# Performance work log

Measured on AMD Instinct MI355X. Metric: run time of the kernel, lower is better.

## Reference

```python
import jax, jax.numpy as jnp
import numpy as np


def _layernorm(x, g, b, eps=1e-5):
    m = jnp.mean(x, axis=-1, keepdims=True)
    v = jnp.var(x, axis=-1, keepdims=True)
    return (x - m) / jnp.sqrt(v + eps) * g + b


def _gat_layer(x, W, a1, a2, Wo, bo, diag_mask):
    # x: [B,N,D]; W: [H,D,D]; a1,a2: [H,D]; Wo: [H*D,D]; bo: [D]
    # Additive-attention split: a.[h_i;h_j] = a1.h_i + a2.h_j (same math as
    # the torch concat+linear, since the score layer is linear and bias-free).
    h = jnp.einsum('bni,hio->bhno', x, W)                       # [B,H,N,D]
    s1 = jnp.einsum('bhnd,hd->bhn', h, a1)                      # [B,H,N]
    s2 = jnp.einsum('bhnd,hd->bhn', h, a2)                      # [B,H,N]
    e = jax.nn.leaky_relu(s1[..., :, None] + s2[..., None, :], 0.2)  # [B,H,N,N]
    # fully-connected adjacency = ones - eye -> mask only the diagonal
    e = jnp.where(diag_mask, -jnp.inf, e)
    alpha = jax.nn.softmax(e, axis=-1)                          # [B,H,N,N]
    out = jnp.einsum('bhij,bhjd->bhid', alpha, h)               # [B,H,N,D]
    B, H, N, D = out.shape
    out = out.transpose(0, 2, 1, 3).reshape(B, N, H * D)        # concat heads
    return out @ Wo + bo                                        # [B,N,D]


def setup_inputs() -> dict:
    key = jax.random.key(0)
    ks = jax.random.split(key, 9)
    B, N, IN, D, H, L = 16, 1024, 7, 128, 4, 3
    s = 0.1
    return {
        'node_features': jax.random.normal(ks[0], (B, N, IN), jnp.float32),
        'Wp': jax.random.normal(ks[1], (IN, D), jnp.float32) * s,
        'bp': jax.random.normal(ks[2], (D,), jnp.float32) * s,
        'W':  jax.random.normal(ks[3], (L, H, D, D), jnp.float32) * s,
        'a1': jax.random.normal(ks[4], (L, H, D), jnp.float32) * s,
        'a2': jax.random.normal(ks[5], (L, H, D), jnp.float32) * s,
        'Wo': jax.random.normal(ks[6], (L, H * D, D), jnp.float32) * s,
        'bo': jax.random.normal(ks[7], (L, D), jnp.float32) * s,
        'gamma': jnp.ones((L, D), jnp.float32),
        'beta': jnp.zeros((L, D), jnp.float32),
    }


def reference(node_features, Wp, bp, W, a1, a2, Wo, bo, gamma, beta):
    B, N, _ = node_features.shape
    L = W.shape[0]
    diag_mask = jnp.eye(N, dtype=bool)  # adjacency==0 positions of (ones-eye)
    x = node_features @ Wp + bp         # input_proj
    for i in range(L):
        x_new = _gat_layer(x, W[i], a1[i], a2[i], Wo[i], bo[i], diag_mask)
        if i > 0:
            x = _layernorm(x + x_new, gamma[i], beta[i])  # residual + LN
        else:
            x = _layernorm(x_new, gamma[i], beta[i])
        if i < L - 1:
            x = jax.nn.relu(x)
    return x
```

## Files before the change

kernel.cpp:

```cpp
#include <hip/hip_runtime.h>
#include <hip/hip_bf16.h>

typedef __attribute__((ext_vector_type(8))) _Float16 f16x8;
typedef __attribute__((ext_vector_type(2))) _Float16 f16x2;
typedef __attribute__((ext_vector_type(8))) short short8;
typedef __attribute__((ext_vector_type(4))) short short4v;
typedef __attribute__((ext_vector_type(4))) float f32x4;

#define LDP 72
#define LDH 64

typedef const __attribute__((address_space(1))) unsigned int* gas_ptr;
typedef __attribute__((address_space(3))) unsigned int* las_ptr;
#define GLDS16(gp, lp) \
  __builtin_amdgcn_global_load_lds((gas_ptr)(gp), (las_ptr)(lp), 16, 0, 0)

#if __has_builtin(__builtin_amdgcn_fdot2)
#define FDOT2(a, b, c) __builtin_amdgcn_fdot2((a), (b), (c), false)
#else
__device__ __forceinline__ float FDOT2(f16x2 a, f16x2 b, float c) {
  return c + (float)a[0] * (float)b[0] + (float)a[1] * (float)b[1];
}
#endif

union h8u {
  f16x8 v;
  f16x2 h[4];
};

__device__ __forceinline__ short f2h(float f) {
  union { _Float16 h; short s; } u; u.h = (_Float16)f; return u.s;
}
__device__ __forceinline__ float h2f(short s) {
  union { short s; _Float16 h; } u; u.s = s; return (float)u.h;
}

__global__ __launch_bounds__(256) void k_tw(const float* __restrict__ W,
                                            const float* __restrict__ Wo,
                                            short* __restrict__ WT,
                                            short* __restrict__ WoT) {
  int idx = blockIdx.x * 256 + threadIdx.x;
  if (idx < 3 * 512 * 128) {
    int l = idx >> 16, rem = idx & 65535;
    int c = rem >> 7, k = rem & 127;
    int h = c >> 7, o = c & 127;
    WT[idx] = f2h(W[(((l * 4 + h) * 128 + k) << 7) + o]);
  } else {
    int j = idx - 3 * 512 * 128;
    int l = j >> 16, rem = j & 65535;
    int d = rem >> 9, c = rem & 511;
    WoT[j] = f2h(Wo[((l * 512 + c) << 7) + d]);
  }
}

__global__ __launch_bounds__(256) void k_inproj(const float* __restrict__ nf,
                                                const float* __restrict__ Wp,
                                                const float* __restrict__ bp,
                                                short* __restrict__ xh) {
  int idx = blockIdx.x * 256 + threadIdx.x;
  int bn = idx >> 7, d = idx & 127;
  float acc = bp[d];
  const float* nr = nf + bn * 7;
#pragma unroll
  for (int i = 0; i < 7; ++i) acc += nr[i] * Wp[(i << 7) + d];
  xh[idx] = f2h(acc);
}

__global__ __launch_bounds__(256) void k_gemm_h(const short* __restrict__ xh,
                                                const short* __restrict__ WT,
                                                short* __restrict__ hT,
                                                const float* __restrict__ a1,
                                                const float* __restrict__ a2,
                                                float* __restrict__ s1g,
                                                float* __restrict__ s2g) {
  __shared__ __align__(16) short As[128 * LDP];
  __shared__ __align__(16) short Bs[128 * LDP];
  __shared__ float sred[2][2][128];
  const int t = threadIdx.x;
  const int bn0 = blockIdx.x << 7;
  const int head = blockIdx.y;
  const int c0 = head << 7;
  const int w = t >> 6, lane = t & 63, lr = lane & 15, lq = lane >> 4;
  const int wr = w >> 1, wc = w & 1;
  f32x4 acc[4][4] = {};
  for (int k0 = 0; k0 < 128; k0 += 64) {
    const int row = t >> 1, half = (t & 1) << 5;
    {
      const short* sa = xh + ((bn0 + row) << 7) + k0 + half;
      short* da = As + row * LDP + half;
      *(short8*)(da) = *(const short8*)(sa);
      *(short8*)(da + 8) = *(const short8*)(sa + 8);
      *(short8*)(da + 16) = *(const short8*)(sa + 16);
      *(short8*)(da + 24) = *(const short8*)(sa + 24);
      const short* sb = WT + ((c0 + row) << 7) + k0 + half;
      short* db = Bs + row * LDP + half;
      *(short8*)(db) = *(const short8*)(sb);
      *(short8*)(db + 8) = *(const short8*)(sb + 8);
      *(short8*)(db + 16) = *(const short8*)(sb + 16);
      *(short8*)(db + 24) = *(const short8*)(sb + 24);
    }
    __syncthreads();
#pragma unroll
    for (int kk = 0; kk < 2; ++kk) {
      f16x8 a[4], b[4];
#pragma unroll
      for (int m = 0; m < 4; ++m)
        a[m] = *(const f16x8*)(As + (wr * 64 + m * 16 + lr) * LDP + (kk << 5) + (lq << 3));
#pragma unroll
      for (int n = 0; n < 4; ++n)
        b[n] = *(const f16x8*)(Bs + (wc * 64 + n * 16 + lr) * LDP + (kk << 5) + (lq << 3));
#pragma unroll
      for (int m = 0; m < 4; ++m)
#pragma unroll
        for (int n = 0; n < 4; ++n)
          acc[m][n] = __builtin_amdgcn_mfma_f32_16x16x32_f16(a[m], b[n], acc[m][n], 0, 0, 0);
    }
    __syncthreads();
  }
  const int b = bn0 >> 10;
  const int nb = bn0 & 1023;
  float a1v[4], a2v[4];
#pragma unroll
  for (int n = 0; n < 4; ++n) {
    int d = wc * 64 + n * 16 + lr;
    a1v[n] = a1[(head << 7) + d];
    a2v[n] = a2[(head << 7) + d];
  }
#pragma unroll
  for (int m = 0; m < 4; ++m)
#pragma unroll
    for (int r = 0; r < 4; ++r) {
      float v1 = 0.f, v2 = 0.f;
#pragma unroll
      for (int n = 0; n < 4; ++n) {
        v1 += acc[m][n][r] * a1v[n];
        v2 += acc[m][n][r] * a2v[n];
      }
#pragma unroll
      for (int off = 1; off < 16; off <<= 1) {
        v1 += __shfl_xor(v1, off);
        v2 += __shfl_xor(v2, off);
      }
      if (lr == 0) {
        int row = wr * 64 + m * 16 + (lq << 2) + r;
        sred[wc][0][row] = v1;
        sred[wc][1][row] = v2;
      }
    }
#pragma unroll
  for (int m = 0; m < 4; ++m) {
    int nrow = nb + wr * 64 + m * 16 + (lq << 2);
#pragma unroll
    for (int n = 0; n < 4; ++n) {
      int d = wc * 64 + n * 16 + lr;
      long base = ((long)((((b << 2) + head) << 7) + d) << 10) + nrow;
      short4v v;
      v[0] = f2h(acc[m][n][0]); v[1] = f2h(acc[m][n][1]);
      v[2] = f2h(acc[m][n][2]); v[3] = f2h(acc[m][n][3]);
      *(short4v*)(hT + base) = v;
    }
  }
  __syncthreads();
  {
    const int bh_ = (b << 2) + head;
    if (t < 128)
      s1g[(bh_ << 10) + nb + t] = sred[0][0][t] + sred[1][0][t];
    else
      s2g[(bh_ << 10) + nb + (t - 128)] = sred[0][1][t - 128] + sred[1][1][t - 128];
  }
}

__global__ __launch_bounds__(256) void k_ef(const float* __restrict__ s2g,
                                            float* __restrict__ s2m,
                                            short* __restrict__ Eh,
                                            short* __restrict__ Fh) {
  const int bh = blockIdx.x, t = threadIdx.x;
  __shared__ float red[4];
  f32x4 v = *(const f32x4*)&s2g[(bh << 10) + (t << 2)];
  float mx = fmaxf(fmaxf(v[0], v[1]), fmaxf(v[2], v[3]));
#pragma unroll
  for (int off = 1; off < 64; off <<= 1) mx = fmaxf(mx, __shfl_xor(mx, off));
  if ((t & 63) == 0) red[t >> 6] = mx;
  __syncthreads();
  const float smax = fmaxf(fmaxf(red[0], red[1]), fmaxf(red[2], red[3]));
  if (t == 0) s2m[bh] = smax;
  short4v e, f;
#pragma unroll
  for (int q = 0; q < 4; ++q) {
    e[q] = f2h(__expf(v[q] - smax));
    f[q] = f2h(__expf(0.2f * (v[q] - smax)));
  }
  *(short4v*)&Eh[(bh << 10) + (t << 2)] = e;
  *(short4v*)&Fh[(bh << 10) + (t << 2)] = f;
}

__global__ __launch_bounds__(256) void k_attn(const short* __restrict__ hT,
                                              const float* __restrict__ s1,
                                              const short* __restrict__ Eh,
                                              const short* __restrict__ Fh,
                                              const float* __restrict__ s2max,
                                              short* __restrict__ attn) {
  __shared__ __align__(16) short Hs[3][128 * LDH];
  __shared__ __align__(16) _Float16 Esh[1024];
  __shared__ __align__(16) _Float16 Fsh[1024];
  const int bh = blockIdx.x, it = blockIdx.y;
  const int i0 = it << 7;
  const int t = threadIdx.x;
  const int w = t >> 6, lane = t & 63, lr = lane & 15, lq = lane >> 4;

  const short* hTb = hT + ((long)bh << 17);
  const int grow = (w << 5) + (lane >> 3);
  const int gcol = ((lane & 7) ^ (lane >> 3)) << 3;
  const short* gsrc = hTb + ((long)grow << 10) + gcol;

#define STAGE(buf, J0)                                             \
  do {                                                             \
    short* ldsb = &Hs[buf][(w << 5) << 6];                         \
    _Pragma("unroll") for (int i_ = 0; i_ < 4; ++i_)               \
        GLDS16(gsrc + ((long)(i_ << 3) << 10) + (J0),              \
               ldsb + ((i_ << 3) << 6));                           \
  } while (0)

  STAGE(0, 0);
  STAGE(1, 64);
  *(short4v*)&Esh[t << 2] = *(const short4v*)&Eh[(bh << 10) + (t << 2)];
  *(short4v*)&Fsh[t << 2] = *(const short4v*)&Fh[(bh << 10) + (t << 2)];

  const float smax = s2max[bh];
  f16x8 Ai8[2], Bi8[2];
  const f16x2 one2 = {(_Float16)1.f, (_Float16)1.f};
  f16x8 dmask[2];
  float dsum[2] = {0.f, 0.f};
#pragma unroll
  for (int m = 0; m < 2; ++m) {
    const int rblk = (w << 5) + (m << 4) + lr;
    float s1v = s1[(bh << 10) + i0 + rblk];
    float x = s1v + smax;
    float mi = fmaxf(x, 0.2f * x);
    _Float16 A_ = (_Float16)__expf(x - mi);
    _Float16 B_ = (_Float16)__expf(0.2f * x - mi);
#pragma unroll
    for (int e = 0; e < 8; ++e) { Ai8[m][e] = A_; Bi8[m][e] = B_; }
    const int lqz = ((m << 1) + (lr >> 3)) & 3, ez = lr & 7;
#pragma unroll
    for (int e = 0; e < 8; ++e)
      dmask[m][e] = (lq == lqz && e == ez) ? (_Float16)0.f : (_Float16)1.f;
  }
  const int jtd = (it << 1) + (w >> 1);
  const int kkd = w & 1;
  f32x4 acc[2][8] = {};
  __syncthreads();

#define TILE(buf, jt, DIAG)                                                    \
  do {                                                                         \
    _Pragma("unroll") for (int kk = 0; kk < 2; ++kk) {                         \
      const int ebase = ((jt) << 6) + (kk << 5) + (lq << 3);                   \
      f16x8 ev8 = *(const f16x8*)&Esh[ebase];                                  \
      f16x8 fv8 = *(const f16x8*)&Fsh[ebase];                                  \
      f16x8 bf[8];                                                             \
      _Pragma("unroll") for (int n = 0; n < 8; ++n) {                          \
        const int r_ = (n << 4) + lr;                                          \
        const int slot_ = ((kk << 2) + lq) ^ (r_ & 7);                         \
        bf[n] = *(const f16x8*)(&Hs[buf][(r_ << 6) + (slot_ << 3)]);           \
      }                                                                        \
      f16x8 af[2];                                                             \
      _Pragma("unroll") for (int m = 0; m < 2; ++m) {                          \
        f16x8 pm = __builtin_elementwise_max(Ai8[m] * ev8, Bi8[m] * fv8);      \
        if ((DIAG) && kk == kkd) pm = pm * dmask[m];                           \
        af[m] = pm;                                                            \
        h8u u_; u_.v = pm;                                                     \
        _Pragma("unroll") for (int p = 0; p < 4; ++p)                          \
            dsum[m] = FDOT2(u_.h[p], one2, dsum[m]);                           \
      }                                                                        \
      _Pragma("unroll") for (int m = 0; m < 2; ++m)                            \
        _Pragma("unroll") for (int n = 0; n < 8; ++n)                          \
            acc[m][n] = __builtin_amdgcn_mfma_f32_16x16x32_f16(                \
                af[m], bf[n], acc[m][n], 0, 0, 0);                             \
    }                                                                          \
  } while (0)

  int cur = 0;
#pragma unroll 1
  for (int jt = 0; jt < 16; ++jt) {
    if (jt < 14) {
      STAGE((cur == 0 ? 2 : cur - 1), (jt + 2) << 6);
      asm volatile("s_waitcnt vmcnt(8)" ::: "memory");
    } else if (jt == 14) {
      asm volatile("s_waitcnt vmcnt(4)" ::: "memory");
    } else {
      asm volatile("s_waitcnt vmcnt(0)" ::: "memory");
    }
    __builtin_amdgcn_s_barrier();
    __builtin_amdgcn_s_setprio(1);
    TILE(cur, jt, jt == jtd);
    __builtin_amdgcn_s_setprio(0);
    __builtin_amdgcn_s_barrier();
    cur = (cur == 2) ? 0 : cur + 1;
  }

  const int b = bh >> 2, head = bh & 3;
#pragma unroll
  for (int m = 0; m < 2; ++m) {
    float s = dsum[m];
    s += __shfl_xor(s, 16);
    s += __shfl_xor(s, 32);
    float rs = 1.f / s;
    f32x4 d4;
#pragma unroll
    for (int q = 0; q < 4; ++q)
      d4[q] = __shfl(rs, (lane & 48) | ((lq << 2) + q));
    int irow = i0 + (w << 5) + (m << 4) + (lq << 2);
#pragma unroll
    for (int n = 0; n < 8; ++n) {
      int d = (n << 4) + lr;
      long base = ((long)((b << 10) + irow) << 9) + (head << 7) + d;
      attn[base] = f2h(acc[m][n][0] * d4[0]);
      attn[base + 512] = f2h(acc[m][n][1] * d4[1]);
      attn[base + 1024] = f2h(acc[m][n][2] * d4[2]);
      attn[base + 1536] = f2h(acc[m][n][3] * d4[3]);
    }
  }
#undef STAGE
#undef TILE
}

template <int HAS_RES, int DO_RELU, int WRITE_OUT>
__global__ __launch_bounds__(256) void k_outproj(const short* __restrict__ attn,
                                                 const short* __restrict__ WoT,
                                                 const float* __restrict__ bo,
                                                 const float* __restrict__ gamma,
                                                 const float* __restrict__ beta,
                                                 float* __restrict__ xf,
                                                 short* __restrict__ xh,
                                                 float* __restrict__ outp) {
  __shared__ __align__(16) short As[32 * LDP];
  __shared__ __align__(16) short Bs[128 * LDP];
  __shared__ float sredS[2][32], sredQ[2][32];
  const int t = threadIdx.x;
  const int bn0 = blockIdx.x << 5;
  const int w = t >> 6, lane = t & 63, lr = lane & 15, lq = lane >> 4;
  const int wm = w & 1, wn = w >> 1;
  f32x4 acc[4] = {};
  const int rowA = t >> 3, chA = (t & 7) << 3;
  const int rowB = t >> 1, chB = (t & 1) << 5;
  for (int k0 = 0; k0 < 512; k0 += 64) {
    {
      const short* sa = attn + ((long)(bn0 + rowA) << 9) + k0 + chA;
      *(short8*)(As + rowA * LDP + chA) = *(const short8*)(sa);
      const short* sb = WoT + (rowB << 9) + k0 + chB;
      short* db = Bs + rowB * LDP + chB;
      *(short8*)(db) = *(const short8*)(sb);
      *(short8*)(db + 8) = *(const short8*)(sb + 8);
      *(short8*)(db + 16) = *(const short8*)(sb + 16);
      *(short8*)(db + 24) = *(const short8*)(sb + 24);
    }
    __syncthreads();
#pragma unroll
    for (int kk = 0; kk < 2; ++kk) {
      f16x8 a = *(const f16x8*)(As + ((wm << 4) + lr) * LDP + (kk << 5) + (lq << 3));
#pragma unroll
      for (int nn = 0; nn < 4; ++nn) {
        f16x8 b = *(const f16x8*)(Bs + ((wn << 6) + (nn << 4) + lr) * LDP + (kk << 5) + (lq << 3));
        acc[nn] = __builtin_amdgcn_mfma_f32_16x16x32_f16(a, b, acc[nn], 0, 0, 0);
      }
    }
    __syncthreads();
  }
  float v[4][4], gam[4], bet[4];
#pragma unroll
  for (int nn = 0; nn < 4; ++nn) {
    int d = (wn << 6) + (nn << 4) + lr;
    float bv = bo[d];
    gam[nn] = gamma[d];
    bet[nn] = beta[d];
#pragma unroll
    for (int r = 0; r < 4; ++r) {
      float x = acc[nn][r] + bv;
      if (HAS_RES) x += xf[((bn0 + (wm << 4) + (lq << 2) + r) << 7) + d];
      v[nn][r] = x;
    }
  }
#pragma unroll
  for (int r = 0; r < 4; ++r) {
    float s = 0.f, q = 0.f;
#pragma unroll
    for (int nn = 0; nn < 4; ++nn) { s += v[nn][r]; q += v[nn][r] * v[nn][r]; }
#pragma unroll
    for (int mk = 1; mk < 16; mk <<= 1) { s += __shfl_xor(s, mk); q += __shfl_xor(q, mk); }
    if (lr == 0) {
      int row = (wm << 4) + (lq << 2) + r;
      sredS[wn][row] = s;
      sredQ[wn][row] = q;
    }
  }
  __syncthreads();
#pragma unroll
  for (int r = 0; r < 4; ++r) {
    int rloc = (wm << 4) + (lq << 2) + r;
    float S = sredS[0][rloc] + sredS[1][rloc];
    float Q = sredQ[0][rloc] + sredQ[1][rloc];
    float mean = S * 0.0078125f;
    float var = Q * 0.0078125f - mean * mean;
    float rstd = rsqrtf(var + 1e-5f);
    int row = bn0 + rloc;
#pragma unroll
    for (int nn = 0; nn < 4; ++nn) {
      int d = (wn << 6) + (nn << 4) + lr;
      float o = (v[nn][r] - mean) * rstd * gam[nn] + bet[nn];
      if (DO_RELU) o = fmaxf(o, 0.f);
      if (WRITE_OUT) {
        outp[(row << 7) + d] = o;
      } else {
        xh[(row << 7) + d] = f2h(o);
        xf[(row << 7) + d] = o;
      }
    }
  }
}

extern "C" void kernel_launch(void* const* d_in, const int* in_sizes, int n_in,
                              void* d_out, int out_size, void* d_ws, size_t ws_size,
                              hipStream_t stream) {
  const float* nf = (const float*)d_in[0];
  const float* Wp = (const float*)d_in[1];
  const float* bp = (const float*)d_in[2];
  const float* W = (const float*)d_in[3];
  const float* a1 = (const float*)d_in[4];
  const float* a2 = (const float*)d_in[5];
  const float* Wo = (const float*)d_in[6];
  const float* bo = (const float*)d_in[7];
  const float* gamma = (const float*)d_in[8];
  const float* beta = (const float*)d_in[9];
  float* outp = (float*)d_out;

  char* ws = (char*)d_ws;
  short* xh = (short*)(ws);
  float* xf = (float*)(ws + (4ll << 20));
  short* hT = (short*)(ws + (12ll << 20));
  short* attn = (short*)(ws + (28ll << 20));
  float* s1 = (float*)(ws + (44ll << 20));
  float* s2g = (float*)(ws + (44ll << 20) + (256ll << 10));
  short* Eh = (short*)(ws + (44ll << 20) + (512ll << 10));
  short* Fh = (short*)(ws + (44ll << 20) + (640ll << 10));
  float* s2m = (float*)(ws + (44ll << 20) + (768ll << 10));
  short* WT = (short*)(ws + (45ll << 20));
  short* WoT = (short*)(ws + (45ll << 20) + 393216);

  k_tw<<<1536, 256, 0, stream>>>(W, Wo, WT, WoT);
  k_inproj<<<8192, 256, 0, stream>>>(nf, Wp, bp, xh);
  for (int l = 0; l < 3; ++l) {
    k_gemm_h<<<dim3(128, 4), 256, 0, stream>>>(xh, WT + l * 65536, hT,
                                               a1 + l * 512, a2 + l * 512, s1, s2g);
    k_ef<<<64, 256, 0, stream>>>(s2g, s2m, Eh, Fh);
    k_attn<<<dim3(64, 8), 256, 0, stream>>>(hT, s1, Eh, Fh, s2m, attn);
    if (l == 0)
      k_outproj<0, 1, 0><<<512, 256, 0, stream>>>(attn, WoT + l * 65536, bo + l * 128,
                                                  gamma + l * 128, beta + l * 128, xf, xh, outp);
    else if (l == 1)
      k_outproj<1, 1, 0><<<512, 256, 0, stream>>>(attn, WoT + l * 65536, bo + l * 128,
                                                  gamma + l * 128, beta + l * 128, xf, xh, outp);
    else
      k_outproj<1, 0, 1><<<512, 256, 0, stream>>>(attn, WoT + l * 65536, bo + l * 128,
                                                  gamma + l * 128, beta + l * 128, xf, xh, outp);
  }
}
```

Baseline: 163.8 us.

## Load attention B operands directly to registers with 2x2 wave tiling

The attention kernel no longer stages hT tiles into LDS through a triple-buffered global_load_lds pipeline with barriers. Each wave now loads its B fragments straight from global memory into registers, double-buffered across pairs of j-tiles. The wave layout changes from 4x1 (32 rows by all 128 columns) to 2x2 (64 rows by 64 columns). This removes the LDS traffic and block barriers, but each wave redoes the P-matrix exp/max work for twice as many rows. It also depends on global-load latency being hidden by a single tile of register prefetch.

```diff
diff --git a/kernel.cpp b/kernel.cpp
--- a/kernel.cpp
+++ b/kernel.cpp
@@ -8,12 +8,6 @@
 typedef __attribute__((ext_vector_type(4))) float f32x4;
 
 #define LDP 72
-#define LDH 64
-
-typedef const __attribute__((address_space(1))) unsigned int* gas_ptr;
-typedef __attribute__((address_space(3))) unsigned int* las_ptr;
-#define GLDS16(gp, lp) \
-  __builtin_amdgcn_global_load_lds((gas_ptr)(gp), (las_ptr)(lp), 16, 0, 0)
 
 #if __has_builtin(__builtin_amdgcn_fdot2)
 #define FDOT2(a, b, c) __builtin_amdgcn_fdot2((a), (b), (c), false)
@@ -200,40 +194,27 @@
                                               const short* __restrict__ Fh,
                                               const float* __restrict__ s2max,
                                               short* __restrict__ attn) {
-  __shared__ __align__(16) short Hs[3][128 * LDH];
   __shared__ __align__(16) _Float16 Esh[1024];
   __shared__ __align__(16) _Float16 Fsh[1024];
   const int bh = blockIdx.x, it = blockIdx.y;
   const int i0 = it << 7;
   const int t = threadIdx.x;
   const int w = t >> 6, lane = t & 63, lr = lane & 15, lq = lane >> 4;
+  const int wm = w & 1, wn = w >> 1;
 
   const short* hTb = hT + ((long)bh << 17);
-  const int grow = (w << 5) + (lane >> 3);
-  const int gcol = ((lane & 7) ^ (lane >> 3)) << 3;
-  const short* gsrc = hTb + ((long)grow << 10) + gcol;
-
-#define STAGE(buf, J0)                                             \
-  do {                                                             \
-    short* ldsb = &Hs[buf][(w << 5) << 6];                         \
-    _Pragma("unroll") for (int i_ = 0; i_ < 4; ++i_)               \
-        GLDS16(gsrc + ((long)(i_ << 3) << 10) + (J0),              \
-               ldsb + ((i_ << 3) << 6));                           \
-  } while (0)
-
-  STAGE(0, 0);
-  STAGE(1, 64);
+  const short* gb = hTb + ((long)((wn << 6) + lr) << 10) + (lq << 3);
+
   *(short4v*)&Esh[t << 2] = *(const short4v*)&Eh[(bh << 10) + (t << 2)];
   *(short4v*)&Fsh[t << 2] = *(const short4v*)&Fh[(bh << 10) + (t << 2)];
 
   const float smax = s2max[bh];
-  f16x8 Ai8[2], Bi8[2];
+  f16x8 Ai8[4], Bi8[4], dmask[4];
   const f16x2 one2 = {(_Float16)1.f, (_Float16)1.f};
-  f16x8 dmask[2];
-  float dsum[2] = {0.f, 0.f};
-#pragma unroll
-  for (int m = 0; m < 2; ++m) {
-    const int rblk = (w << 5) + (m << 4) + lr;
+  float dsum[4] = {0.f, 0.f, 0.f, 0.f};
+#pragma unroll
+  for (int m = 0; m < 4; ++m) {
+    const int rblk = (wm << 6) + (m << 4) + lr;
     float s1v = s1[(bh << 10) + i0 + rblk];
     float x = s1v + smax;
     float mi = fmaxf(x, 0.2f * x);
@@ -246,61 +227,55 @@
     for (int e = 0; e < 8; ++e)
       dmask[m][e] = (lq == lqz && e == ez) ? (_Float16)0.f : (_Float16)1.f;
   }
-  const int jtd = (it << 1) + (w >> 1);
-  const int kkd = w & 1;
-  f32x4 acc[2][8] = {};
+  const int jtd = (it << 1) + wm;
+  f32x4 acc[4][4] = {};
   __syncthreads();
 
-#define TILE(buf, jt, DIAG)                                                    \
-  do {                                                                         \
-    _Pragma("unroll") for (int kk = 0; kk < 2; ++kk) {                         \
-      const int ebase = ((jt) << 6) + (kk << 5) + (lq << 3);                   \
-      f16x8 ev8 = *(const f16x8*)&Esh[ebase];                                  \
-      f16x8 fv8 = *(const f16x8*)&Fsh[ebase];                                  \
-      f16x8 bf[8];                                                             \
-      _Pragma("unroll") for (int n = 0; n < 8; ++n) {                          \
-        const int r_ = (n << 4) + lr;                                          \
-        const int slot_ = ((kk << 2) + lq) ^ (r_ & 7);                         \
-        bf[n] = *(const f16x8*)(&Hs[buf][(r_ << 6) + (slot_ << 3)]);           \
-      }                                                                        \
-      f16x8 af[2];                                                             \
-      _Pragma("unroll") for (int m = 0; m < 2; ++m) {                          \
-        f16x8 pm = __builtin_elementwise_max(Ai8[m] * ev8, Bi8[m] * fv8);      \
-        if ((DIAG) && kk == kkd) pm = pm * dmask[m];                           \
-        af[m] = pm;                                                            \
-        h8u u_; u_.v = pm;                                                     \
-        _Pragma("unroll") for (int p = 0; p < 4; ++p)                          \
-            dsum[m] = FDOT2(u_.h[p], one2, dsum[m]);                           \
-      }                                                                        \
-      _Pragma("unroll") for (int m = 0; m < 2; ++m)                            \
-        _Pragma("unroll") for (int n = 0; n < 8; ++n)                          \
-            acc[m][n] = __builtin_amdgcn_mfma_f32_16x16x32_f16(                \
-                af[m], bf[n], acc[m][n], 0, 0, 0);                             \
-    }                                                                          \
+#define LOADB(B, jt)                                                         \
+  do {                                                                       \
+    _Pragma("unroll") for (int kk = 0; kk < 2; ++kk)                         \
+    _Pragma("unroll") for (int n = 0; n < 4; ++n)                            \
+        B[kk][n] = *(const f16x8*)(gb + ((long)(n << 4) << 10) +             \
+                                   ((jt) << 6) + (kk << 5));                 \
   } while (0)
 
-  int cur = 0;
+#define COMPUTE(B, jt, DIAG)                                                 \
+  do {                                                                       \
+    _Pragma("unroll") for (int kk = 0; kk < 2; ++kk) {                       \
+      const int ebase = ((jt) << 6) + (kk << 5) + (lq << 3);                 \
+      f16x8 ev8 = *(const f16x8*)&Esh[ebase];                                \
+      f16x8 fv8 = *(const f16x8*)&Fsh[ebase];                                \
+      _Pragma("unroll") for (int m = 0; m < 4; ++m) {                        \
+        f16x8 pm = __builtin_elementwise_max(Ai8[m] * ev8, Bi8[m] * fv8);    \
+        if ((DIAG) && kk == (m >> 1)) pm = pm * dmask[m];                    \
+        h8u u_; u_.v = pm;                                                   \
+        _Pragma("unroll") for (int p = 0; p < 4; ++p)                        \
+            dsum[m] = FDOT2(u_.h[p], one2, dsum[m]);                         \
+        _Pragma("unroll") for (int n = 0; n < 4; ++n)                        \
+            acc[m][n] = __builtin_amdgcn_mfma_f32_16x16x32_f16(              \
+                pm, B[kk][n], acc[m][n], 0, 0, 0);                           \
+      }                                                                      \
+    }                                                                        \
+  } while (0)
+
+  f16x8 BA[2][4], BB[2][4];
+  LOADB(BA, 0);
 #pragma unroll 1
-  for (int jt = 0; jt < 16; ++jt) {
-    if (jt < 14) {
-      STAGE((cur == 0 ? 2 : cur - 1), (jt + 2) << 6);
-      asm volatile("s_waitcnt vmcnt(8)" ::: "memory");
-    } else if (jt == 14) {
-      asm volatile("s_waitcnt vmcnt(4)" ::: "memory");
-    } else {
-      asm volatile("s_waitcnt vmcnt(0)" ::: "memory");
-    }
-    __builtin_amdgcn_s_barrier();
+  for (int jt2 = 0; jt2 < 8; ++jt2) {
+    const int jA = jt2 << 1, jB = jA | 1;
+    LOADB(BB, jB);
     __builtin_amdgcn_s_setprio(1);
-    TILE(cur, jt, jt == jtd);
+    COMPUTE(BA, jA, jA == jtd);
     __builtin_amdgcn_s_setprio(0);
-    __builtin_amdgcn_s_barrier();
-    cur = (cur == 2) ? 0 : cur + 1;
+    if (jt2 < 7) LOADB(BA, jA + 2);
+    __builtin_amdgcn_s_setprio(1);
+    COMPUTE(BB, jB, jB == jtd);
+    __builtin_amdgcn_s_setprio(0);
   }
 
   const int b = bh >> 2, head = bh & 3;
 #pragma unroll
-  for (int m = 0; m < 2; ++m) {
+  for (int m = 0; m < 4; ++m) {
     float s = dsum[m];
     s += __shfl_xor(s, 16);
     s += __shfl_xor(s, 32);
@@ -309,10 +284,10 @@
 #pragma unroll
     for (int q = 0; q < 4; ++q)
       d4[q] = __shfl(rs, (lane & 48) | ((lq << 2) + q));
-    int irow = i0 + (w << 5) + (m << 4) + (lq << 2);
-#pragma unroll
-    for (int n = 0; n < 8; ++n) {
-      int d = (n << 4) + lr;
+    int irow = i0 + (wm << 6) + (m << 4) + (lq << 2);
+#pragma unroll
+    for (int n = 0; n < 4; ++n) {
+      int d = (wn << 6) + (n << 4) + lr;
       long base = ((long)((b << 10) + irow) << 9) + (head << 7) + d;
       attn[base] = f2h(acc[m][n][0] * d4[0]);
       attn[base + 512] = f2h(acc[m][n][1] * d4[1]);
@@ -320,8 +295,8 @@
       attn[base + 1536] = f2h(acc[m][n][3] * d4[3]);
     }
   }
-#undef STAGE
-#undef TILE
+#undef LOADB
+#undef COMPUTE
 }
 
 template <int HAS_RES, int DO_RELU, int WRITE_OUT>
```

Measured after the change: 207.0 us. 26.4% more time.
